# Performance work log

Hardware: AMD Instinct MI355X
Metric: run time of the kernel (lower is better)

The kernel has to match this reference:

```python
import math
import jax
import jax.numpy as jnp
import numpy as np

KS = 7  # kernel_size


def _make_cdt_kernel():
    # kornia.create_meshgrid(k,k,normalized=False) -> coords; centered; hypot -> exp(d/-0.35)
    r = np.arange(KS, dtype=np.float32) - (KS // 2)
    yy, xx = np.meshgrid(r, r, indexing="ij")
    k = np.exp(np.hypot(xx, yy) / -0.35)
    return jnp.asarray(k, jnp.float32)[None, None]  # (1,1,KS,KS) OIHW


def setup_inputs() -> dict:
    key = jax.random.key(0)
    B, C, H, W = 32, 3, 256, 256
    u = jax.random.uniform(key, (B, C, H, W), dtype=jnp.float32)
    image = (u < 0.005).astype(jnp.float32)
    return {"image": image}


def reference(image):
    B, C, H, W = image.shape
    kernel = _make_cdt_kernel()
    n_iters = math.ceil(max(H, W) / (KS // 2))  # static
    x = image.reshape(B * C, 1, H, W)
    out0 = jnp.zeros_like(x)

    def step(carry, i):
        out, boundary = carry
        conv = jax.lax.conv_general_dilated(
            boundary, kernel, (1, 1), "SAME",
            dimension_numbers=("NCHW", "OIHW", "NCHW"))
        # -0.35*log(conv) with posinf (conv==0) replaced by 0, exactly as
        # torch.nan_to_num(cdt, posinf=0.0); safe-log form avoids inf/nan.
        pos = conv > 0
        cdt = jnp.where(pos, -0.35 * jnp.log(jnp.where(pos, conv, 1.0)), 0.0)
        mask = cdt > 0
        offset = i.astype(jnp.float32) * (KS / 2)  # i * kernel_size / 2 (true div)
        out = out + jnp.where(mask, offset + cdt, 0.0)
        boundary = jnp.where(mask, 1.0, boundary)
        return (out, boundary), None

    (out, _), _ = jax.lax.scan(step, (out0, x), jnp.arange(n_iters))
    return out.reshape(B, C, H, W)
```

## Files before the change

### kernel.cpp

```cpp
#include <hip/hip_runtime.h>


typedef unsigned short u16x4 __attribute__((ext_vector_type(4)));
typedef unsigned int u32x2 __attribute__((ext_vector_type(2)));
typedef union { u16x4 v; unsigned int d[2]; } U16U;

#define BIGV (1 << 20)
#define GUARD 12
#define ROWB ((GUARD + 256 + GUARD) * 2)
#define CHB (256 * ROWB)

__global__ __launch_bounds__(256) void k_rowdist(const float* __restrict__ img,
                                                 unsigned char* __restrict__ d1) {
  const int lane = threadIdx.x & 63;
  const int wv = threadIdx.x >> 6;
  const int row = blockIdx.x * 4 + wv;
  const int x0 = lane * 4;

  const float4 v = *reinterpret_cast<const float4*>(&img[(size_t)row * 256 + x0]);

  int c0 = (v.x != 0.0f) ? -x0 : BIGV;
  int c1 = (v.y != 0.0f) ? -(x0 + 1) : BIGV;
  int c2 = (v.z != 0.0f) ? -(x0 + 2) : BIGV;
  int c3 = (v.w != 0.0f) ? -(x0 + 3) : BIGV;
  const int p0 = c0;
  const int p1 = min(c1, p0);
  const int p2 = min(c2, p1);
  const int p3 = min(c3, p2);
  int incl = p3;
#pragma unroll
  for (int off = 1; off < 64; off <<= 1) {
    int o = __shfl_up(incl, off, 64);
    if (lane >= off) incl = min(incl, o);
  }
  int excl = __shfl_up(incl, 1, 64);
  if (lane == 0) excl = BIGV;
  const int df0 = x0 + min(p0, excl);
  const int df1 = x0 + 1 + min(p1, excl);
  const int df2 = x0 + 2 + min(p2, excl);
  const int df3 = x0 + 3 + min(p3, excl);

  int g0 = (v.x != 0.0f) ? x0 : BIGV;
  int g1 = (v.y != 0.0f) ? (x0 + 1) : BIGV;
  int g2 = (v.z != 0.0f) ? (x0 + 2) : BIGV;
  int g3 = (v.w != 0.0f) ? (x0 + 3) : BIGV;
  const int q3 = g3;
  const int q2 = min(g2, q3);
  const int q1 = min(g1, q2);
  const int q0 = min(g0, q1);
  int incl2 = q0;
#pragma unroll
  for (int off = 1; off < 64; off <<= 1) {
    int o = __shfl_down(incl2, off, 64);
    if (lane < 64 - off) incl2 = min(incl2, o);
  }
  int excl2 = __shfl_down(incl2, 1, 64);
  if (lane == 63) excl2 = BIGV;
  const int db0 = min(q0, excl2) - x0;
  const int db1 = min(q1, excl2) - (x0 + 1);
  const int db2 = min(q2, excl2) - (x0 + 2);
  const int db3 = min(q3, excl2) - (x0 + 3);

  const unsigned int d0 = (unsigned int)min(min(df0, db0), 127);
  const unsigned int d1v = (unsigned int)min(min(df1, db1), 127);
  const unsigned int d2 = (unsigned int)min(min(df2, db2), 127);
  const unsigned int d3 = (unsigned int)min(min(df3, db3), 127);
  const int ch = row >> 8, y = row & 255;
  const size_t base = (size_t)ch * CHB + (size_t)y * ROWB;

  u32x2 pk;
  pk.x = d0 | (d1v << 16);
  pk.y = d2 | (d3 << 16);
  *reinterpret_cast<u32x2*>(&d1[base + 2 * GUARD + 2 * x0]) = pk;

  u32x2 gv;
  gv.x = 0x007F007Fu;
  gv.y = 0x007F007Fu;
  if (lane < 3)
    *reinterpret_cast<u32x2*>(&d1[base + lane * 8]) = gv;
  else if (lane >= 61)
    *reinterpret_cast<u32x2*>(&d1[base + 536 + (lane - 61) * 8]) = gv;
}

#define TAPROW(s_, t_, A0, A1, A2, A3, A4, A5, A6)                              \
  do {                                                                          \
    const unsigned int r0_ = R[(s_) + (t_)][0];                                 \
    const unsigned int r1_ = R[(s_) + (t_)][1];                                 \
    const unsigned int r2_ = R[(s_) + (t_)][2];                                 \
    A0 += (((__builtin_amdgcn_alignbyte(r1_, r0_, 1) + Cp) & 0x80808080u) >> 7);\
    A1 += (((__builtin_amdgcn_alignbyte(r1_, r0_, 2) + Cp) & 0x80808080u) >> 7);\
    A2 += (((__builtin_amdgcn_alignbyte(r1_, r0_, 3) + Cp) & 0x80808080u) >> 7);\
    A3 += (((r1_ + Cp) & 0x80808080u) >> 7);                                    \
    A4 += (((__builtin_amdgcn_alignbyte(r2_, r1_, 1) + Cp) & 0x80808080u) >> 7);\
    A5 += (((__builtin_amdgcn_alignbyte(r2_, r1_, 2) + Cp) & 0x80808080u) >> 7);\
    A6 += (((__builtin_amdgcn_alignbyte(r2_, r1_, 3) + Cp) & 0x80808080u) >> 7);\
  } while (0)

#define TAPROWC(s_, t_, A0, A1, A2, A4, A5, A6)   \
  do {                                                                          \
    const unsigned int r0_ = R[(s_) + (t_)][0];                                 \
    const unsigned int r1_ = R[(s_) + (t_)][1];                                 \
    const unsigned int r2_ = R[(s_) + (t_)][2];                                 \
    A0 += (((__builtin_amdgcn_alignbyte(r1_, r0_, 1) + Cp) & 0x80808080u) >> 7);\
    A1 += (((__builtin_amdgcn_alignbyte(r1_, r0_, 2) + Cp) & 0x80808080u) >> 7);\
    A2 += (((__builtin_amdgcn_alignbyte(r1_, r0_, 3) + Cp) & 0x80808080u) >> 7);\
    A4 += (((__builtin_amdgcn_alignbyte(r2_, r1_, 1) + Cp) & 0x80808080u) >> 7);\
    A5 += (((__builtin_amdgcn_alignbyte(r2_, r1_, 2) + Cp) & 0x80808080u) >> 7);\
    A6 += (((__builtin_amdgcn_alignbyte(r2_, r1_, 3) + Cp) & 0x80808080u) >> 7);\
  } while (0)

#define EPI(s_)                                                                 \
  do {                                                                          \
    const unsigned int Dc = R[(s_) + 3][1];                                     \
    U16U u_;                                                                    \
    u_.d[0] = __builtin_amdgcn_perm(0u, Dc, 0x0C010C00u);                       \
    u_.d[1] = __builtin_amdgcn_perm(0u, Dc, 0x0C030C02u);                       \
    const u16x4 V = __builtin_elementwise_max(u_.v, kOne);                      \
    const u16x4 I16 = ((V - kOne) * k86) >> k8;       \
    U16U ci_, ii_;                                                              \
    ii_.v = I16;                                                                \
    ci_.v = k127 - (u16x4)(I16 + I16 + I16);                                    \
    const unsigned int Cp =                                                     \
        __builtin_amdgcn_perm(ci_.d[1], ci_.d[0], 0x06040200u);                 \
    unsigned int aA = 0, aB = 0, aC = 0, aD = 0;                                \
    TAPROW(s_, 0, aD, aD, aC, aC, aC, aD, aD);                                  \
    TAPROW(s_, 1, aD, aC, aB, aB, aB, aC, aD);                                  \
    TAPROW(s_, 2, aC, aB, aA, aA, aA, aB, aC);                                  \
    TAPROWC(s_, 3, aC, aB, aA, aA, aB, aC);                                     \
    TAPROW(s_, 4, aC, aB, aA, aA, aA, aB, aC);                                  \
    TAPROW(s_, 5, aD, aC, aB, aB, aB, aC, aD);                                  \
    TAPROW(s_, 6, aD, aD, aC, aC, aC, aD, aD);                                  \
    float4 res4;                                                                \
    float* rp = &res4.x;                                                        \
    const unsigned int iw0 = ii_.d[0], iw1 = ii_.d[1];                          \
    _Pragma("unroll") for (int k = 0; k < 4; ++k) {                             \
      const float fa = (float)((aA >> (8 * k)) & 255u);                         \
      const float fb = (float)((aB >> (8 * k)) & 255u);                         \
      const float fc = (float)((aC >> (8 * k)) & 255u);                         \
      const float fd = (float)((aD >> (8 * k)) & 255u);                         \
      const float conv =                                                        \
          W4 - (fa * wA + fb * wB + fc * wC + fd * wD);                         \
      const unsigned int ik = (k < 2) ? ((iw0 >> (16 * k)) & 0xFFFFu)           \
                                      : ((iw1 >> (16 * (k - 2))) & 0xFFFFu);    \
      const unsigned int dk = (Dc >> (8 * k)) & 255u;                           \
      const float r =                                                           \
          fmaf(3.5f, (float)ik, -0.35f * __logf(fmaxf(conv, 1e-30f)));          \
      rp[k] = (dk > 0u && conv > 1e-6f) ? r : 0.0f;                             \
    }                                                                           \
    *reinterpret_cast<float4*>(&out[obase + (size_t)(s_) * 256]) = res4;        \
  } while (0)

__global__ __launch_bounds__(256, 6) void k_fused(const unsigned char* __restrict__ d1,
                                                  float* __restrict__ out) {
  const int ch = blockIdx.z;
  const int yt = blockIdx.y;
  const int xt = blockIdx.x;
  const int x0 = xt * 32;
  const int y0 = yt * 128;
  const int tid = threadIdx.x;
  const int lastxt = (int)gridDim.x - 1;

  __shared__ __align__(16) unsigned char s1[256 * 80];
  __shared__ __align__(16) unsigned char Ds[134 * 44];

  const unsigned char* src = d1 + (size_t)ch * CHB + 2 * x0 + 2 * (GUARD - 4);
#pragma unroll
  for (int it = 0; it < 5; ++it) {
    const int idx = it * 256 + tid;
    const int y = (idx * 13108) >> 16;
    const int seg = idx - y * 5;
    *reinterpret_cast<uint4*>(&s1[y * 80 + seg * 16]) =
        *reinterpret_cast<const uint4*>(&src[y * ROWB + seg * 16]);
  }
  __syncthreads();

  const int ybot = 255 * 80;
#pragma unroll 1
  for (int it = 0; it < 6; ++it) {
    const int idx = it * 256 + tid;
    if (idx >= 1340) break;
    const int r = (idx * 6554) >> 16;
    const int g = idx - r * 10;
    const int y = y0 + r - 3;
    const bool ghost =
        (xt == 0 && g == 0) || (xt == lastxt && g == 9) || y < 0 || y > 255;
    if (ghost) {
      *reinterpret_cast<unsigned int*>(&Ds[r * 44 + g * 4]) = 0x7F7F7F7Fu;
      continue;
    }
    const int g8 = g * 8;
    const int rb = y * 80 + g8;
    u16x4 b = *reinterpret_cast<const u16x4*>(&s1[rb]);
    int au = rb, ad = rb;
#pragma unroll
    for (int k = 1; k <= 8; ++k) {
      au = max(au - 80, g8);
      ad = min(ad + 80, ybot + g8);
      const u16x4 u = *reinterpret_cast<const u16x4*>(&s1[au]);
      const u16x4 w = *reinterpret_cast<const u16x4*>(&s1[ad]);
      const unsigned short ks = (unsigned short)k;
      const u16x4 kk = {ks, ks, ks, ks};
      b = __builtin_elementwise_min(b, __builtin_elementwise_max(u, kk));
      b = __builtin_elementwise_min(b, __builtin_elementwise_max(w, kk));
    }
    int bm = max(max((int)b.x, (int)b.y), max((int)b.z, (int)b.w));
    int k = 9;
    while (k < bm) {
#pragma unroll
      for (int j = 0; j < 4; ++j) {
        const unsigned short ks = (unsigned short)(k + j);
        au = max(au - 80, g8);
        ad = min(ad + 80, ybot + g8);
        const u16x4 u = *reinterpret_cast<const u16x4*>(&s1[au]);
        const u16x4 w = *reinterpret_cast<const u16x4*>(&s1[ad]);
        const u16x4 kk = {ks, ks, ks, ks};
        b = __builtin_elementwise_min(b, __builtin_elementwise_max(u, kk));
        b = __builtin_elementwise_min(b, __builtin_elementwise_max(w, kk));
      }
      k += 4;
      bm = max(max((int)b.x, (int)b.y), max((int)b.z, (int)b.w));
    }
    union { u16x4 v; u32x2 d; } cc;
    cc.v = b;
    const unsigned int packed = __builtin_amdgcn_perm(cc.d.y, cc.d.x, 0x06040200u);
    *reinterpret_cast<unsigned int*>(&Ds[r * 44 + g * 4]) = packed;
  }
  __syncthreads();

  const float wA = 3.17814e-2f, wB = 2.35426e-3f, wC = 1.91126e-4f, wD = 1.35150e-5f;
  const float W4 = 8.0f * wA + 12.0f * wB + 16.0f * wC + 12.0f * wD;
  const u16x4 kOne = {1, 1, 1, 1};
  const u16x4 k86 = {86, 86, 86, 86};
  const u16x4 k8 = {8, 8, 8, 8};
  const u16x4 k127 = {127, 127, 127, 127};

  const int cg = tid & 7;
  const int rg = tid >> 3;
  const int rl0 = rg * 4;
  const int jb = cg * 4;
  const size_t obase = (size_t)ch * 65536 + (size_t)(y0 + rl0) * 256 + x0 + cg * 4;

  unsigned int R[10][3];
#pragma unroll
  for (int u = 0; u < 10; ++u) {
    const unsigned char* p = &Ds[(rl0 + u) * 44 + jb];
    R[u][0] = *reinterpret_cast<const unsigned int*>(p);
    R[u][1] = *reinterpret_cast<const unsigned int*>(p + 4);
    R[u][2] = *reinterpret_cast<const unsigned int*>(p + 8);
  }

  EPI(0); EPI(1); EPI(2); EPI(3);
}

extern "C" void kernel_launch(void* const* d_in, const int* in_sizes, int n_in,
                              void* d_out, int out_size, void* d_ws, size_t ws_size,
                              hipStream_t stream) {
  const float* img = (const float*)d_in[0];
  float* out = (float*)d_out;
  unsigned char* Dbuf = (unsigned char*)d_ws;

  const int total = in_sizes[0];
  const int nch = total >> 16;

  k_rowdist<<<dim3(nch * 64), dim3(256), 0, stream>>>(img, Dbuf);
  k_fused<<<dim3(8, 2, nch), dim3(256), 0, stream>>>(Dbuf, out);
}
```

Before: 45.80 us.

## Store row distances as bytes and widen in LDS; flatten column min-search

The row-distance pass now writes one byte per pixel, with 8-byte guards, instead of 16-bit values with 12-entry guards. This halves the intermediate buffer traffic. The fused kernel loads the byte rows and widens them to 16-bit in shared memory with perm ops, using a padded 96-byte row stride. The vertical min search is restructured into independent loads and tree reductions to expose ILP, and the occupancy hint drops from 6 to 5 blocks because shared memory use grows.

```diff
diff --git a/kernel.cpp b/kernel.cpp
--- a/kernel.cpp
+++ b/kernel.cpp
@@ -6,8 +6,7 @@
 typedef union { u16x4 v; unsigned int d[2]; } U16U;
 
 #define BIGV (1 << 20)
-#define GUARD 12
-#define ROWB ((GUARD + 256 + GUARD) * 2)
+#define ROWB 272
 #define CHB (256 * ROWB)
 
 __global__ __launch_bounds__(256) void k_rowdist(const float* __restrict__ img,
@@ -67,19 +66,12 @@
   const unsigned int d3 = (unsigned int)min(min(df3, db3), 127);
   const int ch = row >> 8, y = row & 255;
   const size_t base = (size_t)ch * CHB + (size_t)y * ROWB;
-
-  u32x2 pk;
-  pk.x = d0 | (d1v << 16);
-  pk.y = d2 | (d3 << 16);
-  *reinterpret_cast<u32x2*>(&d1[base + 2 * GUARD + 2 * x0]) = pk;
-
-  u32x2 gv;
-  gv.x = 0x007F007Fu;
-  gv.y = 0x007F007Fu;
-  if (lane < 3)
-    *reinterpret_cast<u32x2*>(&d1[base + lane * 8]) = gv;
-  else if (lane >= 61)
-    *reinterpret_cast<u32x2*>(&d1[base + 536 + (lane - 61) * 8]) = gv;
+  *reinterpret_cast<unsigned int*>(&d1[base + 8 + x0]) =
+      d0 | (d1v << 8) | (d2 << 16) | (d3 << 24);
+  if (lane < 2)
+    *reinterpret_cast<unsigned int*>(&d1[base + lane * 4]) = 0u;
+  else if (lane >= 62)
+    *reinterpret_cast<unsigned int*>(&d1[base + 264 + (lane - 62) * 4]) = 0u;
 }
 
 #define TAPROW(s_, t_, A0, A1, A2, A3, A4, A5, A6)                              \
@@ -150,7 +142,11 @@
     *reinterpret_cast<float4*>(&out[obase + (size_t)(s_) * 256]) = res4;        \
   } while (0)
 
-__global__ __launch_bounds__(256, 6) void k_fused(const unsigned char* __restrict__ d1,
+#define LDQ(off) (*reinterpret_cast<const u16x4*>(&s1[(off)]))
+#define EMIN __builtin_elementwise_min
+#define EMAX __builtin_elementwise_max
+
+__global__ __launch_bounds__(256, 5) void k_fused(const unsigned char* __restrict__ d1,
                                                   float* __restrict__ out) {
   const int ch = blockIdx.z;
   const int yt = blockIdx.y;
@@ -160,21 +156,33 @@
   const int tid = threadIdx.x;
   const int lastxt = (int)gridDim.x - 1;
 
-  __shared__ __align__(16) unsigned char s1[256 * 80];
+  __shared__ __align__(16) unsigned char s1[256 * 96];
   __shared__ __align__(16) unsigned char Ds[134 * 44];
 
-  const unsigned char* src = d1 + (size_t)ch * CHB + 2 * x0 + 2 * (GUARD - 4);
-#pragma unroll
-  for (int it = 0; it < 5; ++it) {
+  const unsigned char* src = d1 + (size_t)ch * CHB + x0;
+#pragma unroll
+  for (int it = 0; it < 3; ++it) {
     const int idx = it * 256 + tid;
-    const int y = (idx * 13108) >> 16;
-    const int seg = idx - y * 5;
-    *reinterpret_cast<uint4*>(&s1[y * 80 + seg * 16]) =
-        *reinterpret_cast<const uint4*>(&src[y * ROWB + seg * 16]);
+    const int y = (idx * 21846) >> 16;
+    const int seg = idx - y * 3;
+    const uint4 q = *reinterpret_cast<const uint4*>(&src[y * ROWB + seg * 16]);
+    uint4 lo, hi;
+    lo.x = __builtin_amdgcn_perm(0u, q.x, 0x0C010C00u);
+    lo.y = __builtin_amdgcn_perm(0u, q.x, 0x0C030C02u);
+    lo.z = __builtin_amdgcn_perm(0u, q.y, 0x0C010C00u);
+    lo.w = __builtin_amdgcn_perm(0u, q.y, 0x0C030C02u);
+    hi.x = __builtin_amdgcn_perm(0u, q.z, 0x0C010C00u);
+    hi.y = __builtin_amdgcn_perm(0u, q.z, 0x0C030C02u);
+    hi.z = __builtin_amdgcn_perm(0u, q.w, 0x0C010C00u);
+    hi.w = __builtin_amdgcn_perm(0u, q.w, 0x0C030C02u);
+    *reinterpret_cast<uint4*>(&s1[y * 96 + seg * 32]) = lo;
+    *reinterpret_cast<uint4*>(&s1[y * 96 + seg * 32 + 16]) = hi;
   }
   __syncthreads();
 
-  const int ybot = 255 * 80;
+  const u16x4 K1 = {1, 1, 1, 1}, K2 = {2, 2, 2, 2}, K3 = {3, 3, 3, 3},
+              K4 = {4, 4, 4, 4}, K5 = {5, 5, 5, 5}, K6 = {6, 6, 6, 6},
+              K7 = {7, 7, 7, 7}, K8 = {8, 8, 8, 8};
 #pragma unroll 1
   for (int it = 0; it < 6; ++it) {
     const int idx = it * 256 + tid;
@@ -188,35 +196,58 @@
       *reinterpret_cast<unsigned int*>(&Ds[r * 44 + g * 4]) = 0x7F7F7F7Fu;
       continue;
     }
-    const int g8 = g * 8;
-    const int rb = y * 80 + g8;
-    u16x4 b = *reinterpret_cast<const u16x4*>(&s1[rb]);
-    int au = rb, ad = rb;
-#pragma unroll
-    for (int k = 1; k <= 8; ++k) {
-      au = max(au - 80, g8);
-      ad = min(ad + 80, ybot + g8);
-      const u16x4 u = *reinterpret_cast<const u16x4*>(&s1[au]);
-      const u16x4 w = *reinterpret_cast<const u16x4*>(&s1[ad]);
-      const unsigned short ks = (unsigned short)k;
-      const u16x4 kk = {ks, ks, ks, ks};
-      b = __builtin_elementwise_min(b, __builtin_elementwise_max(u, kk));
-      b = __builtin_elementwise_min(b, __builtin_elementwise_max(w, kk));
-    }
+    const int jb = 8 + 8 * g;
+    const int rb = y * 96 + jb;
+    const int bot = 255 * 96 + jb;
+    const u16x4 b0 = LDQ(rb);
+    const u16x4 u1 = LDQ(max(rb - 96, jb));
+    const u16x4 u2 = LDQ(max(rb - 192, jb));
+    const u16x4 u3 = LDQ(max(rb - 288, jb));
+    const u16x4 u4 = LDQ(max(rb - 384, jb));
+    const u16x4 u5 = LDQ(max(rb - 480, jb));
+    const u16x4 u6 = LDQ(max(rb - 576, jb));
+    const u16x4 u7 = LDQ(max(rb - 672, jb));
+    const u16x4 u8 = LDQ(max(rb - 768, jb));
+    const u16x4 w1 = LDQ(min(rb + 96, bot));
+    const u16x4 w2 = LDQ(min(rb + 192, bot));
+    const u16x4 w3 = LDQ(min(rb + 288, bot));
+    const u16x4 w4 = LDQ(min(rb + 384, bot));
+    const u16x4 w5 = LDQ(min(rb + 480, bot));
+    const u16x4 w6 = LDQ(min(rb + 576, bot));
+    const u16x4 w7 = LDQ(min(rb + 672, bot));
+    const u16x4 w8 = LDQ(min(rb + 768, bot));
+    const u16x4 mu = EMIN(EMIN(EMIN(EMAX(u1, K1), EMAX(u2, K2)),
+                                EMIN(EMAX(u3, K3), EMAX(u4, K4))),
+                          EMIN(EMIN(EMAX(u5, K5), EMAX(u6, K6)),
+                                EMIN(EMAX(u7, K7), EMAX(u8, K8))));
+    const u16x4 mw = EMIN(EMIN(EMIN(EMAX(w1, K1), EMAX(w2, K2)),
+                                EMIN(EMAX(w3, K3), EMAX(w4, K4))),
+                          EMIN(EMIN(EMAX(w5, K5), EMAX(w6, K6)),
+                                EMIN(EMAX(w7, K7), EMAX(w8, K8))));
+    u16x4 b = EMIN(b0, EMIN(mu, mw));
     int bm = max(max((int)b.x, (int)b.y), max((int)b.z, (int)b.w));
     int k = 9;
+    int au = rb - 768, ad = rb + 768;
     while (k < bm) {
-#pragma unroll
-      for (int j = 0; j < 4; ++j) {
-        const unsigned short ks = (unsigned short)(k + j);
-        au = max(au - 80, g8);
-        ad = min(ad + 80, ybot + g8);
-        const u16x4 u = *reinterpret_cast<const u16x4*>(&s1[au]);
-        const u16x4 w = *reinterpret_cast<const u16x4*>(&s1[ad]);
-        const u16x4 kk = {ks, ks, ks, ks};
-        b = __builtin_elementwise_min(b, __builtin_elementwise_max(u, kk));
-        b = __builtin_elementwise_min(b, __builtin_elementwise_max(w, kk));
-      }
+      const unsigned short s1k = (unsigned short)(k), s2k = (unsigned short)(k + 1),
+                           s3k = (unsigned short)(k + 2), s4k = (unsigned short)(k + 3);
+      const u16x4 c1 = {s1k, s1k, s1k, s1k}, c2 = {s2k, s2k, s2k, s2k},
+                  c3 = {s3k, s3k, s3k, s3k}, c4 = {s4k, s4k, s4k, s4k};
+      const u16x4 a1 = LDQ(max(au - 96, jb));
+      const u16x4 a2 = LDQ(max(au - 192, jb));
+      const u16x4 a3 = LDQ(max(au - 288, jb));
+      const u16x4 a4 = LDQ(max(au - 384, jb));
+      const u16x4 e1 = LDQ(min(ad + 96, bot));
+      const u16x4 e2 = LDQ(min(ad + 192, bot));
+      const u16x4 e3 = LDQ(min(ad + 288, bot));
+      const u16x4 e4 = LDQ(min(ad + 384, bot));
+      const u16x4 t = EMIN(EMIN(EMIN(EMAX(a1, c1), EMAX(a2, c2)),
+                                 EMIN(EMAX(a3, c3), EMAX(a4, c4))),
+                           EMIN(EMIN(EMAX(e1, c1), EMAX(e2, c2)),
+                                 EMIN(EMAX(e3, c3), EMAX(e4, c4))));
+      b = EMIN(b, t);
+      au -= 384;
+      ad += 384;
       k += 4;
       bm = max(max((int)b.x, (int)b.y), max((int)b.z, (int)b.w));
     }
@@ -237,13 +268,13 @@
   const int cg = tid & 7;
   const int rg = tid >> 3;
   const int rl0 = rg * 4;
-  const int jb = cg * 4;
+  const int jb2 = cg * 4;
   const size_t obase = (size_t)ch * 65536 + (size_t)(y0 + rl0) * 256 + x0 + cg * 4;
 
   unsigned int R[10][3];
 #pragma unroll
   for (int u = 0; u < 10; ++u) {
-    const unsigned char* p = &Ds[(rl0 + u) * 44 + jb];
+    const unsigned char* p = &Ds[(rl0 + u) * 44 + jb2];
     R[u][0] = *reinterpret_cast<const unsigned int*>(p);
     R[u][1] = *reinterpret_cast<const unsigned int*>(p + 4);
     R[u][2] = *reinterpret_cast<const unsigned int*>(p + 8);
```

Result: no change. 45.67 us (-0.3%).
